# Kernel optimization log

Hardware: AMD Instinct MI355X
Metric: run time of the kernel (lower is better)

The kernel has to match this reference:

```python
import jax, jax.numpy as jnp
import numpy as np

N_NODES = 50000
N_EDGES = 800000
N_FEAT = 128
HIDDEN = 64
EMBED = 300
N_CLASSES = 10
N_GRAPHS = 500
LEAKY_SLOPE = 0.01  # torch F.leaky_relu default


def gcn_conv(x, W, b, src, dst, n_nodes):
    # PyG GCNConv: h = x @ W; add self-loops; norm = deg^{-1/2}[src] * deg^{-1/2}[dst]
    h = x @ W  # [N, H]
    deg = jax.ops.segment_sum(jnp.ones_like(dst, dtype=h.dtype), dst, num_segments=n_nodes) + 1.0  # +1 self-loop
    dis = jax.lax.rsqrt(deg)  # deg^{-1/2}, deg >= 1 so finite
    norm = dis[src] * dis[dst]  # [E]
    agg = jax.ops.segment_sum(h[src] * norm[:, None], dst, num_segments=n_nodes)
    agg = agg + h * (dis * dis)[:, None]  # self-loop contribution
    return agg + b


def segment_softmax(s, seg, num_segments):
    # s: [N, 1]; softmax over nodes within each graph
    m = jax.ops.segment_max(s, seg, num_segments=num_segments)
    e = jnp.exp(s - m[seg])
    z = jax.ops.segment_sum(e, seg, num_segments=num_segments)
    return e / z[seg]


def setup_inputs() -> dict:
    key = jax.random.key(0)
    ks = jax.random.split(key, 16)

    def glorot(k, shape):
        fan_in, fan_out = shape[0], shape[1]
        lim = np.sqrt(6.0 / (fan_in + fan_out)).astype(np.float32)
        return jax.random.uniform(k, shape, jnp.float32, -lim, lim)

    x = jax.random.normal(ks[0], (N_NODES, N_FEAT), jnp.float32)
    edge_index = jax.random.randint(ks[1], (2, N_EDGES), 0, N_NODES, dtype=jnp.int64)
    batch = jnp.sort(jax.random.randint(ks[2], (N_NODES,), 0, N_GRAPHS, dtype=jnp.int64))
    return {
        "x": x,
        "edge_index": edge_index,
        "batch": batch,
        "W1": glorot(ks[3], (N_FEAT, HIDDEN)),
        "b1": jnp.zeros((HIDDEN,), jnp.float32),
        "W2": glorot(ks[4], (HIDDEN, HIDDEN)),
        "b2": jnp.zeros((HIDDEN,), jnp.float32),
        "att_w": glorot(ks[5], (HIDDEN, 1)),
        "att_b": jnp.zeros((1,), jnp.float32),
        "proj_w": glorot(ks[6], (HIDDEN, EMBED)),
        "proj_b": jnp.zeros((EMBED,), jnp.float32),
        "cls_w1": glorot(ks[7], (EMBED, 128)),
        "cls_b1": jnp.zeros((128,), jnp.float32),
        "cls_w2": glorot(ks[8], (128, N_CLASSES)),
        "cls_b2": jnp.zeros((N_CLASSES,), jnp.float32),
    }


def reference(x, edge_index, batch, W1, b1, W2, b2, att_w, att_b, proj_w, proj_b, cls_w1, cls_b1, cls_w2, cls_b2):
    src, dst = edge_index[0], edge_index[1]
    n_nodes = x.shape[0]
    h = jax.nn.relu(gcn_conv(x, W1, b1, src, dst, n_nodes))
    # dropout is identity in eval mode
    h = jax.nn.relu(gcn_conv(h, W2, b2, src, dst, n_nodes))  # [N, H]
    att = jax.nn.leaky_relu(h @ att_w + att_b, negative_slope=LEAKY_SLOPE)  # [N, 1]
    att = segment_softmax(att, batch, N_GRAPHS)
    g = jax.ops.segment_sum(att * h, batch, num_segments=N_GRAPHS)  # [G, H]
    g = g @ proj_w + proj_b  # [G, EMBED]
    out = jax.nn.relu(g @ cls_w1 + cls_b1) @ cls_w2 + cls_b2  # [G, num_classes]
    return out
```

## Files before the change

kernel.cpp:

```cpp
#include <hip/hip_runtime.h>
#include <hip/hip_fp16.h>
#include <math.h>

#define N_NODES   50000
#define N_EDGES   800000
#define N_FEAT    128
#define HIDDEN    64
#define EMBED     300
#define N_CLASSES 10
#define N_GRAPHS  500
#define LEAKY     0.01f
#define SCAN_BLOCKS ((N_NODES + 255) / 256)

typedef __attribute__((ext_vector_type(4))) _Float16 half4f;
typedef __attribute__((ext_vector_type(8))) _Float16 half8;
typedef __attribute__((ext_vector_type(4))) float f32x4;

__device__ __forceinline__ float pk_w(unsigned p) {
    return __half2float(__ushort_as_half((unsigned short)(p >> 16)));
}

__global__ void k_zero(int* deg, int* gs, int* ge) {
    int i = blockIdx.x * 256 + threadIdx.x;
    if (i < N_NODES) deg[i] = 0;
    if (i < N_GRAPHS) { gs[i] = 0; ge[i] = 0; }
}

__global__ void k_w1t(const float* __restrict__ W1, __half* __restrict__ W1T) {
    int idx = blockIdx.x * 256 + threadIdx.x;
    if (idx < N_FEAT * HIDDEN) {
        int n = idx >> 7, k = idx & 127;
        W1T[idx] = __float2half(W1[k * HIDDEN + n]);
    }
}

__global__ void k_deg_rank(const int* __restrict__ dst, int* deg, int* rank) {
    int e = blockIdx.x * 256 + threadIdx.x;
    if (e < N_EDGES) rank[e] = atomicAdd(&deg[dst[e]], 1);
}

__global__ __launch_bounds__(256) void k_scan1(const int* __restrict__ deg, int* row_start,
                                               int* partials, float* dis) {
    __shared__ int wsum[4];
    int i = blockIdx.x * 256 + threadIdx.x;
    int v = (i < N_NODES) ? deg[i] : 0;
    int lane = threadIdx.x & 63, wid = threadIdx.x >> 6;
    int s = v;
    #pragma unroll
    for (int off = 1; off < 64; off <<= 1) {
        int t = __shfl_up(s, off, 64);
        if (lane >= off) s += t;
    }
    if (lane == 63) wsum[wid] = s;
    __syncthreads();
    int woff = 0;
    for (int w = 0; w < wid; ++w) woff += wsum[w];
    if (i < N_NODES) {
        row_start[i] = woff + s - v;
        dis[i] = rsqrtf((float)(deg[i] + 1));
    }
    if (threadIdx.x == 255) partials[blockIdx.x] = woff + s;
}

__global__ __launch_bounds__(256) void k_scan2(int* partials) {
    __shared__ int wsum[4];
    int v = (threadIdx.x < SCAN_BLOCKS) ? partials[threadIdx.x] : 0;
    int lane = threadIdx.x & 63, wid = threadIdx.x >> 6;
    int s = v;
    #pragma unroll
    for (int off = 1; off < 64; off <<= 1) {
        int t = __shfl_up(s, off, 64);
        if (lane >= off) s += t;
    }
    if (lane == 63) wsum[wid] = s;
    __syncthreads();
    int woff = 0;
    for (int w = 0; w < wid; ++w) woff += wsum[w];
    if (threadIdx.x < SCAN_BLOCKS) partials[threadIdx.x] = woff + s - v;
}

__global__ void k_scan3(int* row_start, const int* __restrict__ partials) {
    int i = blockIdx.x * 256 + threadIdx.x;
    if (i < N_NODES) row_start[i] += partials[blockIdx.x];
    if (i == 0) row_start[N_NODES] = N_EDGES;
}

__global__ void k_fill(const int* __restrict__ src, const int* __restrict__ dst,
                       const int* __restrict__ rank, const int* __restrict__ row_start,
                       const float* __restrict__ dis, unsigned* __restrict__ pk) {
    int e = blockIdx.x * 256 + threadIdx.x;
    if (e < N_EDGES) {
        int s = src[e], d = dst[e];
        float w = dis[s] * dis[d];
        unsigned short wh = __half_as_ushort(__float2half(w));
        pk[row_start[d] + rank[e]] = (unsigned)s | ((unsigned)wh << 16);
    }
}

__global__ __launch_bounds__(256) void k_gemm1(const float* __restrict__ x,
                                               const __half* __restrict__ W1T,
                                               __half* __restrict__ h) {
    int tid = threadIdx.x, wid = tid >> 6, lane = tid & 63;
    int r16 = lane & 15, kg = lane >> 4;
    int rowbase = blockIdx.x * 64 + wid * 16;
    int arow = rowbase + r16;
    bool avalid = arow < N_NODES;
    const float* xr = x + (size_t)arow * N_FEAT;

    half8 a[4];
    #pragma unroll
    for (int kt = 0; kt < 4; ++kt) {
        int k0 = kt * 32 + kg * 8;
        float4 u = avalid ? *(const float4*)(xr + k0)     : make_float4(0.f, 0.f, 0.f, 0.f);
        float4 v = avalid ? *(const float4*)(xr + k0 + 4) : make_float4(0.f, 0.f, 0.f, 0.f);
        a[kt][0] = (_Float16)u.x; a[kt][1] = (_Float16)u.y;
        a[kt][2] = (_Float16)u.z; a[kt][3] = (_Float16)u.w;
        a[kt][4] = (_Float16)v.x; a[kt][5] = (_Float16)v.y;
        a[kt][6] = (_Float16)v.z; a[kt][7] = (_Float16)v.w;
    }

    #pragma unroll
    for (int nt = 0; nt < 4; ++nt) {
        f32x4 acc = {0.f, 0.f, 0.f, 0.f};
        const _Float16* wp = (const _Float16*)W1T + (size_t)(nt * 16 + r16) * N_FEAT + kg * 8;
        #pragma unroll
        for (int kt = 0; kt < 4; ++kt) {
            half8 b = *(const half8*)(wp + kt * 32);
            acc = __builtin_amdgcn_mfma_f32_16x16x32_f16(a[kt], b, acc, 0, 0, 0);
        }
        int col = nt * 16 + r16;
        #pragma unroll
        for (int r = 0; r < 4; ++r) {
            int row = rowbase + kg * 4 + r;
            if (row < N_NODES) h[(size_t)row * HIDDEN + col] = __float2half(acc[r]);
        }
    }
}

__device__ __forceinline__ void gather4pk(const __half* __restrict__ h,
                                          const unsigned* __restrict__ pk,
                                          int s, int e, int lane, int g4, int q,
                                          float4& acc) {
    for (int cs = s; cs < e; cs += 64) {
        unsigned pkv = (cs + lane < e) ? pk[cs + lane] : 0u;
        int avail = e - cs; if (avail > 64) avail = 64;
        int iters = (avail + 3) >> 2;
        #pragma unroll 2
        for (int t = 0; t < iters; ++t) {
            unsigned p = __shfl(pkv, t * 4 + g4, 64);
            float w = pk_w(p);
            half4f hv = *(const half4f*)(h + ((size_t)(p & 0xFFFFu)) * HIDDEN + (q << 2));
            acc.x = fmaf(w, (float)hv.x, acc.x);
            acc.y = fmaf(w, (float)hv.y, acc.y);
            acc.z = fmaf(w, (float)hv.z, acc.z);
            acc.w = fmaf(w, (float)hv.w, acc.w);
        }
    }
}

__device__ __forceinline__ void xreduce(float4& a) {
    a.x += __shfl_xor(a.x, 16, 64); a.y += __shfl_xor(a.y, 16, 64);
    a.z += __shfl_xor(a.z, 16, 64); a.w += __shfl_xor(a.w, 16, 64);
    a.x += __shfl_xor(a.x, 32, 64); a.y += __shfl_xor(a.y, 32, 64);
    a.z += __shfl_xor(a.z, 32, 64); a.w += __shfl_xor(a.w, 32, 64);
}

__global__ __launch_bounds__(256) void k_gg(const __half* __restrict__ h1,
                                            const unsigned* __restrict__ pk,
                                            const int* __restrict__ row_start,
                                            const float* __restrict__ dis,
                                            const float* __restrict__ b1,
                                            const float* __restrict__ W2,
                                            __half* __restrict__ h2) {
    __shared__ float sW[HIDDEN * HIDDEN];
    __shared__ float sa[16 * HIDDEN];
    {
        const float4* W4 = (const float4*)W2;
        float4* sW4 = (float4*)sW;
        #pragma unroll
        for (int i = 0; i < 4; ++i)
            sW4[i * 256 + threadIdx.x] = W4[i * 256 + threadIdx.x];
    }

    int tid = threadIdx.x, wid = tid >> 6, lane = tid & 63;
    int g4 = lane >> 4, q = lane & 15;
    int base = blockIdx.x * 16 + wid * 4;
    #pragma unroll
    for (int i = 0; i < 4; ++i) {
        int node = base + i;
        int s = row_start[node], e = row_start[node + 1];
        float4 acc = {0.f, 0.f, 0.f, 0.f};
        gather4pk(h1, pk, s, e, lane, g4, q, acc);
        xreduce(acc);
        float dv = dis[node], dd = dv * dv;
        half4f sv = *(const half4f*)(h1 + (size_t)node * HIDDEN + (q << 2));
        float4 bv = *(const float4*)(b1 + (q << 2));
        float4 r;
        r.x = fmaxf(fmaf((float)sv.x, dd, bv.x) + acc.x, 0.f);
        r.y = fmaxf(fmaf((float)sv.y, dd, bv.y) + acc.y, 0.f);
        r.z = fmaxf(fmaf((float)sv.z, dd, bv.z) + acc.z, 0.f);
        r.w = fmaxf(fmaf((float)sv.w, dd, bv.w) + acc.w, 0.f);
        if (g4 == 0) *(float4*)&sa[(wid * 4 + i) * HIDDEN + (q << 2)] = r;
    }
    __syncthreads();

    int f = lane;
    float o0 = 0.f, o1 = 0.f, o2 = 0.f, o3 = 0.f;
    const float* sa0 = &sa[wid * 4 * HIDDEN];
    #pragma unroll 8
    for (int k = 0; k < HIDDEN; ++k) {
        float wv = sW[k * HIDDEN + f];
        o0 = fmaf(sa0[k], wv, o0);
        o1 = fmaf(sa0[HIDDEN + k], wv, o1);
        o2 = fmaf(sa0[2 * HIDDEN + k], wv, o2);
        o3 = fmaf(sa0[3 * HIDDEN + k], wv, o3);
    }
    h2[(size_t)(base + 0) * HIDDEN + f] = __float2half(o0);
    h2[(size_t)(base + 1) * HIDDEN + f] = __float2half(o1);
    h2[(size_t)(base + 2) * HIDDEN + f] = __float2half(o2);
    h2[(size_t)(base + 3) * HIDDEN + f] = __float2half(o3);
}

__global__ __launch_bounds__(256) void k_gather2(const __half* __restrict__ h2,
                                                 const unsigned* __restrict__ pk,
                                                 const int* __restrict__ row_start,
                                                 const float* __restrict__ dis,
                                                 const float* __restrict__ b2,
                                                 const float* __restrict__ att_w,
                                                 const float* __restrict__ att_b,
                                                 float* __restrict__ agg2,
                                                 float* __restrict__ att_s) {
    int tid = threadIdx.x, wid = tid >> 6, lane = tid & 63;
    int g4 = lane >> 4, q = lane & 15;
    int node = blockIdx.x * 4 + wid;
    int s = row_start[node], e = row_start[node + 1];
    float4 acc = {0.f, 0.f, 0.f, 0.f};
    gather4pk(h2, pk, s, e, lane, g4, q, acc);
    xreduce(acc);
    float dv = dis[node], dd = dv * dv;
    half4f sv = *(const half4f*)(h2 + (size_t)node * HIDDEN + (q << 2));
    float4 bv = *(const float4*)(b2 + (q << 2));
    float4 r;
    r.x = fmaxf(fmaf((float)sv.x, dd, bv.x) + acc.x, 0.f);
    r.y = fmaxf(fmaf((float)sv.y, dd, bv.y) + acc.y, 0.f);
    r.z = fmaxf(fmaf((float)sv.z, dd, bv.z) + acc.z, 0.f);
    r.w = fmaxf(fmaf((float)sv.w, dd, bv.w) + acc.w, 0.f);
    if (g4 == 0) *(float4*)(agg2 + (size_t)node * HIDDEN + (q << 2)) = r;

    float4 aw = *(const float4*)(att_w + (q << 2));
    float v = fmaf(r.x, aw.x, fmaf(r.y, aw.y, fmaf(r.z, aw.z, r.w * aw.w)));
    v += __shfl_xor(v, 1, 64); v += __shfl_xor(v, 2, 64);
    v += __shfl_xor(v, 4, 64); v += __shfl_xor(v, 8, 64);
    if (lane == 0) {
        float sc = v + att_b[0];
        att_s[node] = (sc > 0.0f) ? sc : LEAKY * sc;
    }
}

__global__ void k_gbounds(const int* __restrict__ batch, int* gs, int* ge) {
    int n = blockIdx.x * 256 + threadIdx.x;
    if (n < N_NODES) {
        int b = batch[n];
        if (n == 0 || batch[n - 1] != b) gs[b] = n;
        if (n == N_NODES - 1 || batch[n + 1] != b) ge[b] = n + 1;
    }
}

__global__ __launch_bounds__(256) void k_pool_head(const float* __restrict__ agg2,
                                                   const float* __restrict__ att_s,
                                                   const int* __restrict__ gs,
                                                   const int* __restrict__ ge,
                                                   const float* __restrict__ proj_w,
                                                   const float* __restrict__ proj_b,
                                                   const float* __restrict__ cls_w1,
                                                   const float* __restrict__ cls_b1,
                                                   const float* __restrict__ cls_w2,
                                                   const float* __restrict__ cls_b2,
                                                   float* __restrict__ out) {
    __shared__ float red[4];
    __shared__ float red2[4 * 64];
    __shared__ float sG[HIDDEN];
    __shared__ float sT1[EMBED];
    __shared__ float sT2[128];
    int gid = blockIdx.x;
    int tid = threadIdx.x, f = tid & 63, w = tid >> 6;
    int s = gs[gid], e = ge[gid];

    float m = -INFINITY;
    for (int n = s + tid; n < e; n += 256) m = fmaxf(m, att_s[n]);
    #pragma unroll
    for (int o = 32; o > 0; o >>= 1) m = fmaxf(m, __shfl_xor(m, o, 64));
    if (f == 0) red[w] = m;
    __syncthreads();
    m = fmaxf(fmaxf(red[0], red[1]), fmaxf(red[2], red[3]));
    __syncthreads();

    float z = 0.0f;
    for (int n = s + tid; n < e; n += 256) z += expf(att_s[n] - m);
    #pragma unroll
    for (int o = 32; o > 0; o >>= 1) z += __shfl_xor(z, o, 64);
    if (f == 0) red[w] = z;
    __syncthreads();
    z = red[0] + red[1] + red[2] + red[3];
    float inv = (e > s) ? 1.0f / z : 0.0f;

    float acc = 0.0f;
    for (int n = s + w; n < e; n += 4)
        acc = fmaf(expf(att_s[n] - m) * inv, agg2[(size_t)n * HIDDEN + f], acc);
    red2[w * 64 + f] = acc;
    __syncthreads();
    if (w == 0) sG[f] = red2[f] + red2[64 + f] + red2[128 + f] + red2[192 + f];
    __syncthreads();

    for (int c = tid; c < EMBED; c += 256) {
        float a = proj_b[c];
        #pragma unroll 8
        for (int k = 0; k < HIDDEN; ++k) a = fmaf(sG[k], proj_w[k * EMBED + c], a);
        sT1[c] = a;
    }
    __syncthreads();

    if (tid < 128) {
        float a = cls_b1[tid];
        for (int k = 0; k < EMBED; ++k) a = fmaf(sT1[k], cls_w1[k * 128 + tid], a);
        sT2[tid] = fmaxf(a, 0.f);
    }
    __syncthreads();

    if (tid < N_CLASSES) {
        float a = cls_b2[tid];
        #pragma unroll 8
        for (int k = 0; k < 128; ++k) a = fmaf(sT2[k], cls_w2[k * N_CLASSES + tid], a);
        out[gid * N_CLASSES + tid] = a;
    }
}

extern "C" void kernel_launch(void* const* d_in, const int* in_sizes, int n_in,
                              void* d_out, int out_size, void* d_ws, size_t ws_size,
                              hipStream_t stream) {
    const float* x      = (const float*)d_in[0];
    const int*   ei     = (const int*)d_in[1];
    const int*   batch  = (const int*)d_in[2];
    const float* W1     = (const float*)d_in[3];
    const float* b1     = (const float*)d_in[4];
    const float* W2     = (const float*)d_in[5];
    const float* b2     = (const float*)d_in[6];
    const float* att_w  = (const float*)d_in[7];
    const float* att_b  = (const float*)d_in[8];
    const float* proj_w = (const float*)d_in[9];
    const float* proj_b = (const float*)d_in[10];
    const float* cls_w1 = (const float*)d_in[11];
    const float* cls_b1 = (const float*)d_in[12];
    const float* cls_w2 = (const float*)d_in[13];
    const float* cls_b2 = (const float*)d_in[14];
    float* out = (float*)d_out;

    const int* e_src = ei;
    const int* e_dst = ei + N_EDGES;

    float* base = (float*)d_ws;
    size_t o = 0;
    float*    dis       = base + o;              o += 50048;
    int*      deg_i     = (int*)(base + o);      o += 50048;
    int*      row_start = (int*)(base + o);      o += 50080;
    int*      partials  = (int*)(base + o);      o += 256;
    unsigned* pk        = (unsigned*)(base + o); o += 800000;
    __half*   h1        = (__half*)(base + o);   o += 1600000;
    __half*   h2        = (__half*)(base + o);   o += 1600000;
    float*    agg2      = base + o;              o += 3200000;
    int*      rank      = (int*)agg2;
    float*    att_s     = base + o;              o += 50048;
    int*      gs        = (int*)(base + o);      o += 512;
    int*      ge        = (int*)(base + o);      o += 512;
    __half*   W1T       = (__half*)(base + o);   o += 4096;

    const int NB_N    = (N_NODES + 255) / 256;
    const int NB_E    = (N_EDGES + 255) / 256;
    const int NB_GG   = N_NODES / 16;
    const int NB_ROW4 = N_NODES / 4;
    const int NB_M64  = (N_NODES + 63) / 64;

    k_zero<<<NB_N, 256, 0, stream>>>(deg_i, gs, ge);
    k_w1t<<<(N_FEAT * HIDDEN + 255) / 256, 256, 0, stream>>>(W1, W1T);
    k_deg_rank<<<NB_E, 256, 0, stream>>>(e_dst, deg_i, rank);
    k_scan1<<<SCAN_BLOCKS, 256, 0, stream>>>(deg_i, row_start, partials, dis);
    k_scan2<<<1, 256, 0, stream>>>(partials);
    k_scan3<<<SCAN_BLOCKS, 256, 0, stream>>>(row_start, partials);
    k_fill<<<NB_E, 256, 0, stream>>>(e_src, e_dst, rank, row_start, dis, pk);

    k_gemm1<<<NB_M64, 256, 0, stream>>>(x, W1T, h1);
    k_gg<<<NB_GG, 256, 0, stream>>>(h1, pk, row_start, dis, b1, W2, h2);

    k_gather2<<<NB_ROW4, 256, 0, stream>>>(h2, pk, row_start, dis, b2, att_w, att_b,
                                           agg2, att_s);

    k_gbounds<<<NB_N, 256, 0, stream>>>(batch, gs, ge);
    k_pool_head<<<N_GRAPHS, 256, 0, stream>>>(agg2, att_s, gs, ge,
                                              proj_w, proj_b, cls_w1, cls_b1,
                                              cls_w2, cls_b2, out);
}
```

Baseline: 177.1 us.

## Merge small kernels, use MFMA for second GEMM, store agg2 in fp16

Several independent launches are merged into combined kernels by splitting on block index: zero with the weight transposes, edge fill with gemm1, and the layer-2 gather with graph-bounds detection. The two-stage scan fixup is folded into one kernel where each block reduces the preceding partials itself. The per-node 64x64 GEMM in k_gg moves from scalar FMA on a float W2 in shared memory to fp16 MFMA with a pre-transposed W2. agg2 is stored as fp16 to halve the traffic into pooling, at the cost of some precision. The aim is fewer launches and less memory traffic.

```diff
diff --git a/kernel.cpp b/kernel.cpp
--- a/kernel.cpp
+++ b/kernel.cpp
@@ -10,7 +10,9 @@
 #define N_CLASSES 10
 #define N_GRAPHS  500
 #define LEAKY     0.01f
-#define SCAN_BLOCKS ((N_NODES + 255) / 256)
+#define SCAN_BLOCKS 196
+#define NB_FILL   3125
+#define NB_G2     12500
 
 typedef __attribute__((ext_vector_type(4))) _Float16 half4f;
 typedef __attribute__((ext_vector_type(8))) _Float16 half8;
@@ -20,17 +22,22 @@
     return __half2float(__ushort_as_half((unsigned short)(p >> 16)));
 }
 
-__global__ void k_zero(int* deg, int* gs, int* ge) {
-    int i = blockIdx.x * 256 + threadIdx.x;
-    if (i < N_NODES) deg[i] = 0;
-    if (i < N_GRAPHS) { gs[i] = 0; ge[i] = 0; }
-}
-
-__global__ void k_w1t(const float* __restrict__ W1, __half* __restrict__ W1T) {
-    int idx = blockIdx.x * 256 + threadIdx.x;
-    if (idx < N_FEAT * HIDDEN) {
+__global__ void kA(int* deg, int* gs, int* ge,
+                   const float* __restrict__ W1, __half* __restrict__ W1T,
+                   const float* __restrict__ W2, __half* __restrict__ W2T) {
+    int bid = blockIdx.x, tid = threadIdx.x;
+    if (bid < 196) {
+        int i = bid * 256 + tid;
+        if (i < N_NODES) deg[i] = 0;
+        if (i < N_GRAPHS) { gs[i] = 0; ge[i] = 0; }
+    } else if (bid < 228) {
+        int idx = (bid - 196) * 256 + tid;
         int n = idx >> 7, k = idx & 127;
         W1T[idx] = __float2half(W1[k * HIDDEN + n]);
+    } else {
+        int idx = (bid - 228) * 256 + tid;
+        int n = idx >> 6, k = idx & 63;
+        W2T[idx] = __float2half(W2[k * HIDDEN + n]);
     }
 }
 
@@ -62,47 +69,39 @@
     if (threadIdx.x == 255) partials[blockIdx.x] = woff + s;
 }
 
-__global__ __launch_bounds__(256) void k_scan2(int* partials) {
+__global__ __launch_bounds__(256) void k_scan3b(int* row_start, const int* __restrict__ partials) {
     __shared__ int wsum[4];
-    int v = (threadIdx.x < SCAN_BLOCKS) ? partials[threadIdx.x] : 0;
-    int lane = threadIdx.x & 63, wid = threadIdx.x >> 6;
-    int s = v;
-    #pragma unroll
-    for (int off = 1; off < 64; off <<= 1) {
-        int t = __shfl_up(s, off, 64);
-        if (lane >= off) s += t;
-    }
-    if (lane == 63) wsum[wid] = s;
-    __syncthreads();
-    int woff = 0;
-    for (int w = 0; w < wid; ++w) woff += wsum[w];
-    if (threadIdx.x < SCAN_BLOCKS) partials[threadIdx.x] = woff + s - v;
-}
-
-__global__ void k_scan3(int* row_start, const int* __restrict__ partials) {
-    int i = blockIdx.x * 256 + threadIdx.x;
-    if (i < N_NODES) row_start[i] += partials[blockIdx.x];
+    int bid = blockIdx.x, tid = threadIdx.x;
+    int lane = tid & 63, wid = tid >> 6;
+    int v = (tid < SCAN_BLOCKS && tid < bid) ? partials[tid] : 0;
+    #pragma unroll
+    for (int off = 32; off > 0; off >>= 1) v += __shfl_xor(v, off, 64);
+    if (lane == 0) wsum[wid] = v;
+    __syncthreads();
+    int prefix = wsum[0] + wsum[1] + wsum[2] + wsum[3];
+    int i = bid * 256 + tid;
+    if (i < N_NODES) row_start[i] += prefix;
     if (i == 0) row_start[N_NODES] = N_EDGES;
 }
 
-__global__ void k_fill(const int* __restrict__ src, const int* __restrict__ dst,
-                       const int* __restrict__ rank, const int* __restrict__ row_start,
-                       const float* __restrict__ dis, unsigned* __restrict__ pk) {
-    int e = blockIdx.x * 256 + threadIdx.x;
-    if (e < N_EDGES) {
-        int s = src[e], d = dst[e];
-        float w = dis[s] * dis[d];
-        unsigned short wh = __half_as_ushort(__float2half(w));
-        pk[row_start[d] + rank[e]] = (unsigned)s | ((unsigned)wh << 16);
-    }
-}
-
-__global__ __launch_bounds__(256) void k_gemm1(const float* __restrict__ x,
-                                               const __half* __restrict__ W1T,
-                                               __half* __restrict__ h) {
+__global__ __launch_bounds__(256) void kB(const int* __restrict__ src, const int* __restrict__ dst,
+                                          const int* __restrict__ rank, const int* __restrict__ row_start,
+                                          const float* __restrict__ dis, unsigned* __restrict__ pk,
+                                          const float* __restrict__ x, const __half* __restrict__ W1T,
+                                          __half* __restrict__ h1) {
+    if (blockIdx.x < NB_FILL) {
+        int e = blockIdx.x * 256 + threadIdx.x;
+        if (e < N_EDGES) {
+            int s = src[e], d = dst[e];
+            float w = dis[s] * dis[d];
+            unsigned short wh = __half_as_ushort(__float2half(w));
+            pk[row_start[d] + rank[e]] = (unsigned)s | ((unsigned)wh << 16);
+        }
+        return;
+    }
     int tid = threadIdx.x, wid = tid >> 6, lane = tid & 63;
     int r16 = lane & 15, kg = lane >> 4;
-    int rowbase = blockIdx.x * 64 + wid * 16;
+    int rowbase = (blockIdx.x - NB_FILL) * 64 + wid * 16;
     int arow = rowbase + r16;
     bool avalid = arow < N_NODES;
     const float* xr = x + (size_t)arow * N_FEAT;
@@ -118,7 +117,6 @@
         a[kt][4] = (_Float16)v.x; a[kt][5] = (_Float16)v.y;
         a[kt][6] = (_Float16)v.z; a[kt][7] = (_Float16)v.w;
     }
-
     #pragma unroll
     for (int nt = 0; nt < 4; ++nt) {
         f32x4 acc = {0.f, 0.f, 0.f, 0.f};
@@ -132,7 +130,7 @@
         #pragma unroll
         for (int r = 0; r < 4; ++r) {
             int row = rowbase + kg * 4 + r;
-            if (row < N_NODES) h[(size_t)row * HIDDEN + col] = __float2half(acc[r]);
+            if (row < N_NODES) h1[(size_t)row * HIDDEN + col] = __float2half(acc[r]);
         }
     }
 }
@@ -170,18 +168,9 @@
                                             const int* __restrict__ row_start,
                                             const float* __restrict__ dis,
                                             const float* __restrict__ b1,
-                                            const float* __restrict__ W2,
+                                            const __half* __restrict__ W2T,
                                             __half* __restrict__ h2) {
-    __shared__ float sW[HIDDEN * HIDDEN];
-    __shared__ float sa[16 * HIDDEN];
-    {
-        const float4* W4 = (const float4*)W2;
-        float4* sW4 = (float4*)sW;
-        #pragma unroll
-        for (int i = 0; i < 4; ++i)
-            sW4[i * 256 + threadIdx.x] = W4[i * 256 + threadIdx.x];
-    }
-
+    __shared__ __align__(16) __half sa[16 * 72];
     int tid = threadIdx.x, wid = tid >> 6, lane = tid & 63;
     int g4 = lane >> 4, q = lane & 15;
     int base = blockIdx.x * 16 + wid * 4;
@@ -195,41 +184,55 @@
         float dv = dis[node], dd = dv * dv;
         half4f sv = *(const half4f*)(h1 + (size_t)node * HIDDEN + (q << 2));
         float4 bv = *(const float4*)(b1 + (q << 2));
-        float4 r;
-        r.x = fmaxf(fmaf((float)sv.x, dd, bv.x) + acc.x, 0.f);
-        r.y = fmaxf(fmaf((float)sv.y, dd, bv.y) + acc.y, 0.f);
-        r.z = fmaxf(fmaf((float)sv.z, dd, bv.z) + acc.z, 0.f);
-        r.w = fmaxf(fmaf((float)sv.w, dd, bv.w) + acc.w, 0.f);
-        if (g4 == 0) *(float4*)&sa[(wid * 4 + i) * HIDDEN + (q << 2)] = r;
-    }
-    __syncthreads();
-
-    int f = lane;
-    float o0 = 0.f, o1 = 0.f, o2 = 0.f, o3 = 0.f;
-    const float* sa0 = &sa[wid * 4 * HIDDEN];
-    #pragma unroll 8
-    for (int k = 0; k < HIDDEN; ++k) {
-        float wv = sW[k * HIDDEN + f];
-        o0 = fmaf(sa0[k], wv, o0);
-        o1 = fmaf(sa0[HIDDEN + k], wv, o1);
-        o2 = fmaf(sa0[2 * HIDDEN + k], wv, o2);
-        o3 = fmaf(sa0[3 * HIDDEN + k], wv, o3);
-    }
-    h2[(size_t)(base + 0) * HIDDEN + f] = __float2half(o0);
-    h2[(size_t)(base + 1) * HIDDEN + f] = __float2half(o1);
-    h2[(size_t)(base + 2) * HIDDEN + f] = __float2half(o2);
-    h2[(size_t)(base + 3) * HIDDEN + f] = __float2half(o3);
-}
-
-__global__ __launch_bounds__(256) void k_gather2(const __half* __restrict__ h2,
-                                                 const unsigned* __restrict__ pk,
-                                                 const int* __restrict__ row_start,
-                                                 const float* __restrict__ dis,
-                                                 const float* __restrict__ b2,
-                                                 const float* __restrict__ att_w,
-                                                 const float* __restrict__ att_b,
-                                                 float* __restrict__ agg2,
-                                                 float* __restrict__ att_s) {
+        if (g4 == 0) {
+            half4f r;
+            r.x = (_Float16)fmaxf(fmaf((float)sv.x, dd, bv.x) + acc.x, 0.f);
+            r.y = (_Float16)fmaxf(fmaf((float)sv.y, dd, bv.y) + acc.y, 0.f);
+            r.z = (_Float16)fmaxf(fmaf((float)sv.z, dd, bv.z) + acc.z, 0.f);
+            r.w = (_Float16)fmaxf(fmaf((float)sv.w, dd, bv.w) + acc.w, 0.f);
+            *(half4f*)&sa[(wid * 4 + i) * 72 + (q << 2)] = r;
+        }
+    }
+    __syncthreads();
+
+    int r16 = lane & 15, kg = lane >> 4;
+    f32x4 acc = {0.f, 0.f, 0.f, 0.f};
+    const _Float16* wp = (const _Float16*)W2T + (size_t)(wid * 16 + r16) * HIDDEN + kg * 8;
+    #pragma unroll
+    for (int kt = 0; kt < 2; ++kt) {
+        half8 a = *(const half8*)&sa[r16 * 72 + kt * 32 + kg * 8];
+        half8 b = *(const half8*)(wp + kt * 32);
+        acc = __builtin_amdgcn_mfma_f32_16x16x32_f16(a, b, acc, 0, 0, 0);
+    }
+    int col = wid * 16 + r16;
+    int nodebase = blockIdx.x * 16;
+    #pragma unroll
+    for (int r = 0; r < 4; ++r) {
+        int row = nodebase + kg * 4 + r;
+        h2[(size_t)row * HIDDEN + col] = __float2half(acc[r]);
+    }
+}
+
+__global__ __launch_bounds__(256) void kC(const __half* __restrict__ h2,
+                                          const unsigned* __restrict__ pk,
+                                          const int* __restrict__ row_start,
+                                          const float* __restrict__ dis,
+                                          const float* __restrict__ b2,
+                                          const float* __restrict__ att_w,
+                                          const float* __restrict__ att_b,
+                                          __half* __restrict__ agg2,
+                                          float* __restrict__ att_s,
+                                          const int* __restrict__ batch,
+                                          int* gs, int* ge) {
+    if (blockIdx.x >= NB_G2) {
+        int n = (blockIdx.x - NB_G2) * 256 + threadIdx.x;
+        if (n < N_NODES) {
+            int b = batch[n];
+            if (n == 0 || batch[n - 1] != b) gs[b] = n;
+            if (n == N_NODES - 1 || batch[n + 1] != b) ge[b] = n + 1;
+        }
+        return;
+    }
     int tid = threadIdx.x, wid = tid >> 6, lane = tid & 63;
     int g4 = lane >> 4, q = lane & 15;
     int node = blockIdx.x * 4 + wid;
@@ -245,7 +248,12 @@
     r.y = fmaxf(fmaf((float)sv.y, dd, bv.y) + acc.y, 0.f);
     r.z = fmaxf(fmaf((float)sv.z, dd, bv.z) + acc.z, 0.f);
     r.w = fmaxf(fmaf((float)sv.w, dd, bv.w) + acc.w, 0.f);
-    if (g4 == 0) *(float4*)(agg2 + (size_t)node * HIDDEN + (q << 2)) = r;
+    if (g4 == 0) {
+        half4f rh;
+        rh.x = (_Float16)r.x; rh.y = (_Float16)r.y;
+        rh.z = (_Float16)r.z; rh.w = (_Float16)r.w;
+        *(half4f*)(agg2 + (size_t)node * HIDDEN + (q << 2)) = rh;
+    }
 
     float4 aw = *(const float4*)(att_w + (q << 2));
     float v = fmaf(r.x, aw.x, fmaf(r.y, aw.y, fmaf(r.z, aw.z, r.w * aw.w)));
@@ -257,16 +265,7 @@
     }
 }
 
-__global__ void k_gbounds(const int* __restrict__ batch, int* gs, int* ge) {
-    int n = blockIdx.x * 256 + threadIdx.x;
-    if (n < N_NODES) {
-        int b = batch[n];
-        if (n == 0 || batch[n - 1] != b) gs[b] = n;
-        if (n == N_NODES - 1 || batch[n + 1] != b) ge[b] = n + 1;
-    }
-}
-
-__global__ __launch_bounds__(256) void k_pool_head(const float* __restrict__ agg2,
+__global__ __launch_bounds__(256) void k_pool_head(const __half* __restrict__ agg2,
                                                    const float* __restrict__ att_s,
                                                    const int* __restrict__ gs,
                                                    const int* __restrict__ ge,
@@ -306,7 +305,8 @@
 
     float acc = 0.0f;
     for (int n = s + w; n < e; n += 4)
-        acc = fmaf(expf(att_s[n] - m) * inv, agg2[(size_t)n * HIDDEN + f], acc);
+        acc = fmaf(expf(att_s[n] - m) * inv,
+                   __half2float(agg2[(size_t)n * HIDDEN + f]), acc);
     red2[w * 64 + f] = acc;
     __syncthreads();
     if (w == 0) sG[f] = red2[f] + red2[64 + f] + red2[128 + f] + red2[192 + f];
@@ -367,34 +367,29 @@
     unsigned* pk        = (unsigned*)(base + o); o += 800000;
     __half*   h1        = (__half*)(base + o);   o += 1600000;
     __half*   h2        = (__half*)(base + o);   o += 1600000;
-    float*    agg2      = base + o;              o += 3200000;
+    __half*   agg2      = (__half*)(base + o);   o += 1600000;
     int*      rank      = (int*)agg2;
     float*    att_s     = base + o;              o += 50048;
     int*      gs        = (int*)(base + o);      o += 512;
     int*      ge        = (int*)(base + o);      o += 512;
     __half*   W1T       = (__half*)(base + o);   o += 4096;
-
-    const int NB_N    = (N_NODES + 255) / 256;
-    const int NB_E    = (N_EDGES + 255) / 256;
-    const int NB_GG   = N_NODES / 16;
-    const int NB_ROW4 = N_NODES / 4;
-    const int NB_M64  = (N_NODES + 63) / 64;
-
-    k_zero<<<NB_N, 256, 0, stream>>>(deg_i, gs, ge);
-    k_w1t<<<(N_FEAT * HIDDEN + 255) / 256, 256, 0, stream>>>(W1, W1T);
+    __half*   W2T       = (__half*)(base + o);   o += 2048;
+
+    const int NB_E  = (N_EDGES + 255) / 256;
+    const int NB_GG = N_NODES / 16;
+
+    kA<<<244, 256, 0, stream>>>(deg_i, gs, ge, W1, W1T, W2, W2T);
     k_deg_rank<<<NB_E, 256, 0, stream>>>(e_dst, deg_i, rank);
     k_scan1<<<SCAN_BLOCKS, 256, 0, stream>>>(deg_i, row_start, partials, dis);
-    k_scan2<<<1, 256, 0, stream>>>(partials);
-    k_scan3<<<SCAN_BLOCKS, 256, 0, stream>>>(row_start, partials);
-    k_fill<<<NB_E, 256, 0, stream>>>(e_src, e_dst, rank, row_start, dis, pk);
-
-    k_gemm1<<<NB_M64, 256, 0, stream>>>(x, W1T, h1);
-    k_gg<<<NB_GG, 256, 0, stream>>>(h1, pk, row_start, dis, b1, W2, h2);
-
-    k_gather2<<<NB_ROW4, 256, 0, stream>>>(h2, pk, row_start, dis, b2, att_w, att_b,
-                                           agg2, att_s);
-
-    k_gbounds<<<NB_N, 256, 0, stream>>>(batch, gs, ge);
+    k_scan3b<<<SCAN_BLOCKS, 256, 0, stream>>>(row_start, partials);
+
+    kB<<<NB_FILL + 782, 256, 0, stream>>>(e_src, e_dst, rank, row_start, dis, pk, x, W1T, h1);
+
+    k_gg<<<NB_GG, 256, 0, stream>>>(h1, pk, row_start, dis, b1, W2T, h2);
+
+    kC<<<NB_G2 + SCAN_BLOCKS, 256, 0, stream>>>(h2, pk, row_start, dis, b2, att_w, att_b,
+                                                agg2, att_s, batch, gs, ge);
+
     k_pool_head<<<N_GRAPHS, 256, 0, stream>>>(agg2, att_s, gs, ge,
                                               proj_w, proj_b, cls_w1, cls_b1,
                                               cls_w2, cls_b2, out);
```

Result: faster. 163.8 us (-7.5%).
